# Optimization experiments

Measured on AMD Instinct MI355X. Metric: run time of the kernel, lower is better.

Reference implementation:

```python
import jax, jax.numpy as jnp
import numpy as np
import math

DIM = 2048
H = 16
KV = 4
HD = DIM // H  # 128
ROPE_DIM = 64  # head_dim * rope_fraction(0.5), even
ROPE_BASE = 10000.0
EPS_RMS = 1.1920928955078125e-07  # torch fp32 finfo eps (F.rms_norm default)


def rms_norm(t):
    # F.rms_norm over last dim, no weight
    return t * jax.lax.rsqrt(jnp.mean(t * t, axis=-1, keepdims=True) + EPS_RMS)


def rope_tables(seqlen, dtype):
    inv_freq = 1.0 / (ROPE_BASE ** (jnp.arange(0, ROPE_DIM, 2, dtype=jnp.float32) / ROPE_DIM))
    t = jnp.arange(seqlen, dtype=jnp.float32)
    freqs = jnp.outer(t, inv_freq)  # [S, ROPE_DIM//2]
    return jnp.cos(freqs).astype(dtype)[None, None], jnp.sin(freqs).astype(dtype)[None, None]


def apply_partial_rope(x, cos, sin):
    # x: [B, h, S, HD]; rotate first ROPE_DIM dims, pass through the rest
    xr = x[..., :ROPE_DIM]
    half = ROPE_DIM // 2
    x1, x2 = xr[..., :half], xr[..., half:]
    rotated = jnp.concatenate((x1 * cos + x2 * sin, -x1 * sin + x2 * cos), axis=-1)
    return jnp.concatenate((rotated, x[..., ROPE_DIM:]), axis=-1)


def setup_inputs() -> dict:
    key = jax.random.key(0)
    ks = jax.random.split(key, 5)
    B, S = 4, 1024
    x = jax.random.normal(ks[0], (B, S, DIM), dtype=jnp.float32)
    Wq = jax.random.normal(ks[1], (DIM, DIM), dtype=jnp.float32) * 0.02
    Wk = jax.random.normal(ks[2], (KV * HD, DIM), dtype=jnp.float32) * 0.02
    Wv = jax.random.normal(ks[3], (KV * HD, DIM), dtype=jnp.float32) * 0.02
    Wproj = jax.random.normal(ks[4], (DIM, DIM), dtype=jnp.float32) * 0.02
    # causal boolean mask [B, S, S]
    causal = jnp.tril(jnp.ones((S, S), dtype=bool))
    attn_mask = jnp.broadcast_to(causal[None], (B, S, S))
    return {"x": x, "attn_mask": attn_mask, "Wq": Wq, "Wk": Wk, "Wv": Wv, "Wproj": Wproj}


def reference(x, attn_mask, Wq, Wk, Wv, Wproj):
    B, S, D = x.shape
    repeat = H // KV
    q = (x @ Wq.T).reshape(B, S, H, HD).transpose(0, 2, 1, 3)   # [B,H,S,HD]
    k = (x @ Wk.T).reshape(B, S, KV, HD).transpose(0, 2, 1, 3)  # [B,KV,S,HD]
    v = (x @ Wv.T).reshape(B, S, KV, HD).transpose(0, 2, 1, 3)
    q = rms_norm(q)
    k = rms_norm(k)
    cos, sin = rope_tables(S, q.dtype)
    q = apply_partial_rope(q, cos, sin)
    k = apply_partial_rope(k, cos, sin)
    # GQA: expand kv heads
    k_rep = jnp.repeat(k, repeat, axis=1)  # [B,H,S,HD]
    v_rep = jnp.repeat(v, repeat, axis=1)
    bias = jnp.where(attn_mask[:, None], jnp.float32(0.0), jnp.float32(-10000.0)).astype(q.dtype)
    scores = jnp.einsum('bhqd,bhkd->bhqk', q, k_rep) / math.sqrt(HD) + bias
    attn = jax.nn.softmax(scores, axis=-1)
    y = jnp.einsum('bhqk,bhkd->bhqd', attn, v_rep)
    valid = jnp.any(attn_mask, axis=-1)[:, None, :, None].astype(y.dtype)
    y = y * valid
    # xsa: remove component of y along self value vector
    denom = jnp.maximum(jnp.sum(v_rep * v_rep, axis=-1, keepdims=True), 1e-06)
    proj = jnp.sum(y * v_rep, axis=-1, keepdims=True) / denom
    y = y - proj * v_rep
    y = y.transpose(0, 2, 1, 3).reshape(B, S, D)
    return y @ Wproj.T
```

## Files before the change

kernel.cpp:

```cpp
#include <hip/hip_runtime.h>


typedef __attribute__((ext_vector_type(8))) __bf16 bf16x8;
typedef __attribute__((ext_vector_type(4))) __bf16 bf16x4;
typedef __attribute__((ext_vector_type(4))) float f32x4;

static_assert(sizeof(__bf16) == 2, "bf16 size");

#define MFMA16x16x32(a, b, c) __builtin_amdgcn_mfma_f32_16x16x32_bf16((a), (b), (c), 0, 0, 0)

#if __has_builtin(__builtin_amdgcn_exp2f)
#define EXP2(x) __builtin_amdgcn_exp2f(x)
#else
#define EXP2(x) exp2f(x)
#endif

__device__ __forceinline__ void gload_lds16(const void* g, void* l) {
  __builtin_amdgcn_global_load_lds((const __attribute__((address_space(1))) void*)g,
                                   (__attribute__((address_space(3))) void*)l, 16, 0, 0);
}

__global__ __launch_bounds__(256) void prep(const float* __restrict__ x,
                                            const float* __restrict__ wq,
                                            const float* __restrict__ wk,
                                            const float* __restrict__ wv,
                                            const float* __restrict__ wp,
                                            __bf16* __restrict__ xb,
                                            __bf16* __restrict__ wb,
                                            __bf16* __restrict__ wpb,
                                            float2* __restrict__ tab) {
  constexpr int NX = 2097152;
  constexpr int NW1 = 1048576;
  constexpr int NW2 = 262144;
  constexpr int NP = 1048576;
  constexpr int NT = 32768;
  constexpr int TOT = NX + NW1 + 2 * NW2 + NP + NT;
  auto cast4 = [](const float* s, __bf16* d, int i) {
    f32x4 v = ((const f32x4*)s)[i];
    bf16x4 o;
    o[0] = (__bf16)v[0];
    o[1] = (__bf16)v[1];
    o[2] = (__bf16)v[2];
    o[3] = (__bf16)v[3];
    ((bf16x4*)d)[i] = o;
  };
  int i = blockIdx.x * blockDim.x + threadIdx.x;
  const int stride = gridDim.x * blockDim.x;
  for (; i < TOT; i += stride) {
    int j = i;
    if (j < NX) {
      cast4(x, xb, j);
    } else if ((j -= NX) < NW1) {
      cast4(wq, wb, j);
    } else if ((j -= NW1) < NW2) {
      cast4(wk, wb + (size_t)NW1 * 4, j);
    } else if ((j -= NW2) < NW2) {
      cast4(wv, wb + (size_t)(NW1 + NW2) * 4, j);
    } else if ((j -= NW2) < NP) {
      cast4(wp, wpb, j);
    } else {
      j -= NP;
      const int s = j >> 5, jj = j & 31;
      const float inv = powf(10000.0f, -(float)jj * 0.03125f);
      const float ang = (float)s * inv;
      tab[j] = make_float2(cosf(ang), sinf(ang));
    }
  }
}

template <typename CT, bool FUSE>
__global__ __launch_bounds__(256) void gemm_bt(const __bf16* __restrict__ A,
                                               const __bf16* __restrict__ B,
                                               CT* __restrict__ C, int N, int K, int nbn,
                                               const float2* __restrict__ tab,
                                               __bf16* __restrict__ vt) {
  __shared__ __align__(16) __bf16 SM[24576];
  __bf16* Asb = SM;
  __bf16* Bsb = SM + 12288;
  const int nwg = gridDim.x;
  const int id = blockIdx.x;
  const int xid = (id & 7) * (nwg >> 3) + (id >> 3);
  const int bm = xid / nbn;
  const int bn = xid - bm * nbn;
  const int t = threadIdx.x;
  const int l = t & 63, w = t >> 6;
  const int wr = w >> 1, wc = w & 1;
  const int lr = l & 15, lk = l >> 4;
  const __bf16* Ab = A + (size_t)bm * 128 * K;
  const __bf16* Bb = B + (size_t)bn * 128 * K;
  const int srow = t >> 2;
  const int scol = ((t & 3) ^ ((srow >> 1) & 3)) << 3;
  f32x4 acc[4][4] = {};

  auto stage = [&](int kt, int buf) {
    const int k0 = kt << 5;
    gload_lds16(Ab + (size_t)srow * K + k0 + scol, &Asb[buf * 4096 + t * 8]);
    gload_lds16(Ab + (size_t)(srow + 64) * K + k0 + scol, &Asb[buf * 4096 + 2048 + t * 8]);
    gload_lds16(Bb + (size_t)srow * K + k0 + scol, &Bsb[buf * 4096 + t * 8]);
    gload_lds16(Bb + (size_t)(srow + 64) * K + k0 + scol, &Bsb[buf * 4096 + 2048 + t * 8]);
  };

  stage(0, 0);
  stage(1, 1);
  asm volatile("s_waitcnt vmcnt(4)" ::: "memory");
  __builtin_amdgcn_s_barrier();

  const int NT = K >> 5;
  int cur = 0;
  for (int kt = 0; kt < NT; ++kt) {
    if (kt + 2 < NT) {
      int c2 = cur + 2;
      if (c2 >= 3) c2 -= 3;
      stage(kt + 2, c2);
    }

    bf16x8 af[4], bfr[4];
#pragma unroll
    for (int m = 0; m < 4; ++m) {
      const int row = wr * 64 + m * 16 + lr;
      af[m] = *(const bf16x8*)&Asb[cur * 4096 + row * 32 + ((lk ^ ((row >> 1) & 3)) << 3)];
    }
#pragma unroll
    for (int n = 0; n < 4; ++n) {
      const int row = wc * 64 + n * 16 + lr;
      bfr[n] = *(const bf16x8*)&Bsb[cur * 4096 + row * 32 + ((lk ^ ((row >> 1) & 3)) << 3)];
    }
#pragma unroll
    for (int m = 0; m < 4; ++m)
#pragma unroll
      for (int n = 0; n < 4; ++n) acc[m][n] = MFMA16x16x32(af[m], bfr[n], acc[m][n]);

    if (kt + 2 < NT)
      asm volatile("s_waitcnt vmcnt(4)" ::: "memory");
    else
      asm volatile("s_waitcnt vmcnt(0)" ::: "memory");
    __builtin_amdgcn_s_barrier();

    ++cur;
    if (cur == 3) cur = 0;
  }

  if constexpr (FUSE) {
    if (bn < 20) {
      __syncthreads();
      float* Ls = (float*)SM;
      float ssp[4][4];
#pragma unroll
      for (int m = 0; m < 4; ++m)
#pragma unroll
        for (int i = 0; i < 4; ++i) {
          float s = 0.0f;
#pragma unroll
          for (int n = 0; n < 4; ++n) s += acc[m][n][i] * acc[m][n][i];
#pragma unroll
          for (int off = 1; off < 16; off <<= 1) s += __shfl_xor(s, off);
          ssp[m][i] = s;
        }
      if (lr == 0) {
#pragma unroll
        for (int m = 0; m < 4; ++m)
#pragma unroll
          for (int i = 0; i < 4; ++i)
            Ls[wc * 128 + wr * 64 + m * 16 + lk * 4 + i] = ssp[m][i];
      }
      __syncthreads();
      const bool isq = (bn < 16);
      const float qs = isq ? 0.1275174457f : 1.0f;
#pragma unroll
      for (int m = 0; m < 4; ++m) {
#pragma unroll
        for (int i = 0; i < 4; ++i) {
          const int rl = wr * 64 + m * 16 + lk * 4 + i;
          const int rg = bm * 128 + rl;
          const float sc =
              rsqrtf((Ls[rl] + Ls[128 + rl]) * (1.0f / 128.0f) +
                     1.1920928955078125e-07f) *
              qs;
          CT* Cr = C + (size_t)rg * N + bn * 128;
          if (wc == 0) {
            const int s = rg & 1023;
#pragma unroll
            for (int n = 0; n < 2; ++n) {
              const int j = n * 16 + lr;
              const float2 cs = tab[s * 32 + j];
              const float x1 = acc[m][n][i], x2 = acc[m][n + 2][i];
              Cr[j] = (CT)((x1 * cs.x + x2 * cs.y) * sc);
              Cr[j + 32] = (CT)((-x1 * cs.y + x2 * cs.x) * sc);
            }
          } else {
#pragma unroll
            for (int n = 0; n < 4; ++n)
              Cr[64 + n * 16 + lr] = (CT)(acc[m][n][i] * sc);
          }
        }
      }
      return;
    } else {
#pragma unroll
      for (int m = 0; m < 4; ++m) {
        const int row0 = bm * 128 + wr * 64 + m * 16 + lk * 4;
#pragma unroll
        for (int n = 0; n < 4; ++n) {
          const int col = bn * 128 + wc * 64 + n * 16 + lr;
#pragma unroll
          for (int i = 0; i < 4; ++i)
            C[(size_t)(row0 + i) * N + col] = (CT)acc[m][n][i];
        }
      }
      __syncthreads();
      __bf16* T = SM;
#pragma unroll
      for (int m = 0; m < 4; ++m) {
#pragma unroll
        for (int n = 0; n < 4; ++n) {
          const int cl = wc * 64 + n * 16 + lr;
#pragma unroll
          for (int i = 0; i < 4; ++i) {
            const int rl = wr * 64 + m * 16 + lk * 4 + i;
            T[rl * 140 + cl] = (__bf16)acc[m][n][i];
          }
        }
      }
      __syncthreads();
      const int bb = bm >> 3, s0g = (bm & 7) << 7;
      __bf16* dst = vt + (size_t)(bb * 4 + (bn - 20)) * 131072;
#pragma unroll
      for (int r = 0; r < 8; ++r) {
        const int off = r * 2048 + t * 8;
        const int dd = off >> 7, sc = off & 127;
        bf16x8 v;
#pragma unroll
        for (int j = 0; j < 8; ++j) v[j] = T[(sc + j) * 140 + dd];
        *(bf16x8*)&dst[(size_t)dd * 1024 + ((s0g + sc) ^ ((dd & 7) << 3))] = v;
      }
      return;
    }
  }

#pragma unroll
  for (int m = 0; m < 4; ++m) {
    const int row0 = bm * 128 + wr * 64 + m * 16 + lk * 4;
#pragma unroll
    for (int n = 0; n < 4; ++n) {
      const int col = bn * 128 + wc * 64 + n * 16 + lr;
#pragma unroll
      for (int i = 0; i < 4; ++i) C[(size_t)(row0 + i) * N + col] = (CT)acc[m][n][i];
    }
  }
}

__global__ __launch_bounds__(512) void attn_fwd(const __bf16* __restrict__ qkv,
                                                const __bf16* __restrict__ vt,
                                                __bf16* __restrict__ y) {
  const int id = blockIdx.x;
  const int g = (id & 7) | (((id >> 3) & 1) << 3);
  const int b = g >> 2, kvh = g & 3;
  const int hi = (id >> 4) & 3;
  const int pr = (id >> 6) & 3;
  const int h = kvh * 4 + hi;

  const int t = threadIdx.x;
  const int l = t & 63, w = t >> 6;
  const int lr = l & 15, lk = l >> 4;
  const int lr8 = lr & 7;

  __shared__ __bf16 Ks[2][128 * 128];
  __shared__ __bf16 Vs[2][128 * 128];
  __shared__ __bf16 Ps[8][16 * 128];

  const size_t rb = (size_t)b * 1024;
  const __bf16* Kg0 = qkv + rb * 3072 + 2048 + kvh * 128;
  const __bf16* Vtb = vt + (size_t)(b * 4 + kvh) * 128 * 1024;

  const int srow = t >> 4;
  const int scg = t & 15;
  const int kcolg = (scg ^ (srow & 7)) << 3;

  auto stageK = [&](int kv0, int buf) {
#pragma unroll
    for (int r = 0; r < 4; ++r)
      gload_lds16(Kg0 + (size_t)(kv0 + r * 32 + srow) * 3072 + kcolg,
                  &Ks[buf][0] + r * 4096 + t * 8);
  };
  auto stageV = [&](int kv0, int buf) {
#pragma unroll
    for (int r = 0; r < 4; ++r)
      gload_lds16(Vtb + (size_t)(r * 32 + srow) * 1024 + kv0 + scg * 8,
                  &Vs[buf][0] + r * 4096 + t * 8);
  };

  bf16x8 onesb;
#pragma unroll
  for (int j = 0; j < 8; ++j) onesb[j] = (__bf16)1.0f;

#pragma unroll 1
  for (int pass = 0; pass < 2; ++pass) {
    const int qt = pass ? pr : (7 - pr);
    const int q0 = qt << 7;
    const int nt = qt + 1;

    bf16x8 aq[4];
    {
      const __bf16* qrow = qkv + (rb + q0 + w * 16 + lr) * 3072 + h * 128 + lk * 8;
#pragma unroll
      for (int kk = 0; kk < 4; ++kk) aq[kk] = *(const bf16x8*)(qrow + kk * 32);
    }

    float m_i[4], l_i[4];
    f32x4 o[8] = {};
#pragma unroll
    for (int i = 0; i < 4; ++i) {
      m_i[i] = -1e30f;
      l_i[i] = 0.0f;
    }

    const int rowg0 = q0 + w * 16 + lk * 4;

    stageK(0, 0);
    stageV(0, 0);
    __syncthreads();

    for (int tt = 0; tt < nt; ++tt) {
      const int kv0 = tt << 7;
      const int cur = tt & 1;
      if (tt + 1 < nt) {
        stageK(kv0 + 128, cur ^ 1);
        stageV(kv0 + 128, cur ^ 1);
      }

      f32x4 sacc[8] = {};
      __builtin_amdgcn_s_setprio(1);
#pragma unroll
      for (int kk = 0; kk < 4; ++kk) {
#pragma unroll
        for (int n = 0; n < 8; ++n) {
          const bf16x8 bk = *(const bf16x8*)&Ks[cur][(n * 16 + lr) * 128 +
                                                    ((kk * 32 + lk * 8) ^ (lr8 << 3))];
          sacc[n] = MFMA16x16x32(aq[kk], bk, sacc[n]);
        }
      }
      __builtin_amdgcn_s_setprio(0);

      float pm[4];
#pragma unroll
      for (int i = 0; i < 4; ++i) pm[i] = -1e30f;
      if (tt == qt) {
#pragma unroll
        for (int n = 0; n < 8; ++n) {
          const int colg = kv0 + n * 16 + lr;
#pragma unroll
          for (int i = 0; i < 4; ++i) {
            if (colg > rowg0 + i) sacc[n][i] = -1e30f;
            pm[i] = fmaxf(pm[i], sacc[n][i]);
          }
        }
      } else {
#pragma unroll
        for (int n = 0; n < 8; ++n)
#pragma unroll
          for (int i = 0; i < 4; ++i) pm[i] = fmaxf(pm[i], sacc[n][i]);
      }
#pragma unroll
      for (int i = 0; i < 4; ++i) {
        pm[i] = fmaxf(pm[i], __shfl_xor(pm[i], 1));
        pm[i] = fmaxf(pm[i], __shfl_xor(pm[i], 2));
        pm[i] = fmaxf(pm[i], __shfl_xor(pm[i], 4));
        pm[i] = fmaxf(pm[i], __shfl_xor(pm[i], 8));
      }

      const float dm = fmaxf(fmaxf(pm[0] - m_i[0], pm[1] - m_i[1]),
                             fmaxf(pm[2] - m_i[2], pm[3] - m_i[3]));
      if (__any(dm > 8.0f)) {
#pragma unroll
        for (int i = 0; i < 4; ++i) {
          const float mn = fmaxf(m_i[i], pm[i]);
          const float al = EXP2(m_i[i] - mn);
          m_i[i] = mn;
          l_i[i] *= al;
#pragma unroll
          for (int f = 0; f < 8; ++f) o[f][i] *= al;
        }
      }

#pragma unroll
      for (int n = 0; n < 8; ++n) {
#pragma unroll
        for (int i = 0; i < 4; ++i) {
          const float p = EXP2(sacc[n][i] - m_i[i]);
          const int prow = lk * 4 + i;
          Ps[w][prow * 128 + ((n * 16 + lr) ^ ((prow & 7) << 3))] = (__bf16)p;
        }
      }

      f32x4 lsum = {};
      __builtin_amdgcn_s_setprio(1);
#pragma unroll
      for (int ks = 0; ks < 4; ++ks) {
        const bf16x8 pa =
            *(const bf16x8*)&Ps[w][lr * 128 + ((ks * 32 + lk * 8) ^ (lr8 << 3))];
        lsum = MFMA16x16x32(pa, onesb, lsum);
#pragma unroll
        for (int f = 0; f < 8; ++f) {
          const bf16x8 vb = *(const bf16x8*)&Vs[cur][(f * 16 + lr) * 128 +
                                                     ((ks * 32 + lk * 8) ^ (lr8 << 3))];
          o[f] = MFMA16x16x32(pa, vb, o[f]);
        }
      }
      __builtin_amdgcn_s_setprio(0);
#pragma unroll
      for (int i = 0; i < 4; ++i) l_i[i] += lsum[i];

      __syncthreads();
    }

#pragma unroll
    for (int i = 0; i < 4; ++i) {
      const int sg = rowg0 + i;
      const size_t mg = rb + sg;
      const __bf16* vp = qkv + mg * 3072 + 2560 + kvh * 128;
      const float invl = 1.0f / l_i[i];
      float vvv[8], yvv[8];
      float dyv = 0.0f, dvv = 0.0f;
#pragma unroll
      for (int f = 0; f < 8; ++f) {
        const float vf = (float)vp[f * 16 + lr];
        const float yf = o[f][i] * invl;
        vvv[f] = vf;
        yvv[f] = yf;
        dyv += yf * vf;
        dvv += vf * vf;
      }
#pragma unroll
      for (int off = 1; off < 16; off <<= 1) {
        dyv += __shfl_xor(dyv, off);
        dvv += __shfl_xor(dvv, off);
      }
      const float proj = dyv / fmaxf(dvv, 1e-6f);
      __bf16* yp = y + mg * 2048 + h * 128;
#pragma unroll
      for (int f = 0; f < 8; ++f) yp[f * 16 + lr] = (__bf16)(yvv[f] - proj * vvv[f]);
    }
  }
}

extern "C" void kernel_launch(void* const* d_in, const int* in_sizes, int n_in,
                              void* d_out, int out_size, void* d_ws, size_t ws_size,
                              hipStream_t stream) {
  const float* x = (const float*)d_in[0];
  const float* Wq = (const float*)d_in[2];
  const float* Wk = (const float*)d_in[3];
  const float* Wv = (const float*)d_in[4];
  const float* Wp = (const float*)d_in[5];
  float* out = (float*)d_out;

  __bf16* xb = (__bf16*)d_ws;
  __bf16* Wb = xb + (size_t)4096 * 2048;
  __bf16* Wpb = Wb + (size_t)3072 * 2048;
  __bf16* qkv = Wpb + (size_t)2048 * 2048;
  __bf16* yb = qkv + (size_t)4096 * 3072;
  float2* tab = (float2*)(yb + (size_t)4096 * 2048);
  __bf16* vt = (__bf16*)(tab + 32768);

  prep<<<2048, 256, 0, stream>>>(x, Wq, Wk, Wv, Wp, xb, Wb, Wpb, tab);

  gemm_bt<__bf16, true><<<768, 256, 0, stream>>>(xb, Wb, qkv, 3072, 2048, 24, tab, vt);
  attn_fwd<<<256, 512, 0, stream>>>(qkv, vt, yb);
  gemm_bt<float, false><<<512, 256, 0, stream>>>(yb, Wpb, out, 2048, 2048, 16, nullptr,
                                                 nullptr);
}
```

Before: 172.7 us.

## Switch GEMM to double-buffered LDS and split V transpose into halves

The GEMM main loop goes from a 3-stage LDS pipeline with explicit vmcnt waits to a 2-stage double buffer synchronized with __syncthreads, shrinking shared memory from 48KB to 32KB so more workgroups can be resident. The V-transpose epilogue is done in two 64-row halves with a 137-element padded stride to fit the smaller LDS, and it writes with nontemporal stores. The fp32 output path also uses nontemporal stores. In exchange, global-load latency is hidden less because only one stage is prefetched ahead, and the epilogue gains extra barriers.

```diff
diff --git a/kernel.cpp b/kernel.cpp
--- a/kernel.cpp
+++ b/kernel.cpp
@@ -74,9 +74,9 @@
                                                CT* __restrict__ C, int N, int K, int nbn,
                                                const float2* __restrict__ tab,
                                                __bf16* __restrict__ vt) {
-  __shared__ __align__(16) __bf16 SM[24576];
+  __shared__ __align__(16) __bf16 SM[16384];
   __bf16* Asb = SM;
-  __bf16* Bsb = SM + 12288;
+  __bf16* Bsb = SM + 8192;
   const int nwg = gridDim.x;
   const int id = blockIdx.x;
   const int xid = (id & 7) * (nwg >> 3) + (id >> 3);
@@ -101,18 +101,12 @@
   };
 
   stage(0, 0);
-  stage(1, 1);
-  asm volatile("s_waitcnt vmcnt(4)" ::: "memory");
-  __builtin_amdgcn_s_barrier();
+  __syncthreads();
 
   const int NT = K >> 5;
-  int cur = 0;
   for (int kt = 0; kt < NT; ++kt) {
-    if (kt + 2 < NT) {
-      int c2 = cur + 2;
-      if (c2 >= 3) c2 -= 3;
-      stage(kt + 2, c2);
-    }
+    const int cur = kt & 1;
+    if (kt + 1 < NT) stage(kt + 1, cur ^ 1);
 
     bf16x8 af[4], bfr[4];
 #pragma unroll
@@ -130,19 +124,11 @@
 #pragma unroll
       for (int n = 0; n < 4; ++n) acc[m][n] = MFMA16x16x32(af[m], bfr[n], acc[m][n]);
 
-    if (kt + 2 < NT)
-      asm volatile("s_waitcnt vmcnt(4)" ::: "memory");
-    else
-      asm volatile("s_waitcnt vmcnt(0)" ::: "memory");
-    __builtin_amdgcn_s_barrier();
-
-    ++cur;
-    if (cur == 3) cur = 0;
+    __syncthreads();
   }
 
   if constexpr (FUSE) {
     if (bn < 20) {
-      __syncthreads();
       float* Ls = (float*)SM;
       float ssp[4][4];
 #pragma unroll
@@ -207,31 +193,35 @@
             C[(size_t)(row0 + i) * N + col] = (CT)acc[m][n][i];
         }
       }
-      __syncthreads();
       __bf16* T = SM;
-#pragma unroll
-      for (int m = 0; m < 4; ++m) {
-#pragma unroll
-        for (int n = 0; n < 4; ++n) {
-          const int cl = wc * 64 + n * 16 + lr;
-#pragma unroll
-          for (int i = 0; i < 4; ++i) {
-            const int rl = wr * 64 + m * 16 + lk * 4 + i;
-            T[rl * 140 + cl] = (__bf16)acc[m][n][i];
-          }
-        }
-      }
-      __syncthreads();
       const int bb = bm >> 3, s0g = (bm & 7) << 7;
       __bf16* dst = vt + (size_t)(bb * 4 + (bn - 20)) * 131072;
-#pragma unroll
-      for (int r = 0; r < 8; ++r) {
-        const int off = r * 2048 + t * 8;
-        const int dd = off >> 7, sc = off & 127;
-        bf16x8 v;
-#pragma unroll
-        for (int j = 0; j < 8; ++j) v[j] = T[(sc + j) * 140 + dd];
-        *(bf16x8*)&dst[(size_t)dd * 1024 + ((s0g + sc) ^ ((dd & 7) << 3))] = v;
+#pragma unroll 1
+      for (int half = 0; half < 2; ++half) {
+        __syncthreads();
+        if (wr == half) {
+#pragma unroll
+          for (int m = 0; m < 4; ++m)
+#pragma unroll
+            for (int n = 0; n < 4; ++n) {
+              const int cl = wc * 64 + n * 16 + lr;
+#pragma unroll
+              for (int i = 0; i < 4; ++i)
+                T[(m * 16 + lk * 4 + i) * 137 + cl] = (__bf16)acc[m][n][i];
+            }
+        }
+        __syncthreads();
+#pragma unroll
+        for (int r = 0; r < 4; ++r) {
+          const int off = r * 2048 + t * 8;
+          const int dd = off >> 6;
+          const int sc = off & 63;
+          bf16x8 v;
+#pragma unroll
+          for (int j = 0; j < 8; ++j) v[j] = T[(sc + j) * 137 + dd];
+          const int sg = (s0g + half * 64 + sc) ^ ((dd & 7) << 3);
+          __builtin_nontemporal_store(*(f32x4*)&v, (f32x4*)&dst[(size_t)dd * 1024 + sg]);
+        }
       }
       return;
     }
@@ -244,7 +234,13 @@
     for (int n = 0; n < 4; ++n) {
       const int col = bn * 128 + wc * 64 + n * 16 + lr;
 #pragma unroll
-      for (int i = 0; i < 4; ++i) C[(size_t)(row0 + i) * N + col] = (CT)acc[m][n][i];
+      for (int i = 0; i < 4; ++i) {
+        if constexpr (sizeof(CT) == 4)
+          __builtin_nontemporal_store((CT)acc[m][n][i],
+                                      &C[(size_t)(row0 + i) * N + col]);
+        else
+          C[(size_t)(row0 + i) * N + col] = (CT)acc[m][n][i];
+      }
     }
   }
 }
```

New measurement: 186.4 us. +7.9%, slower.
